# Performance work log

Measured on AMD Instinct MI355X. Metric: run time of the kernel, lower is better.

Reference implementation:

```python
import jax, jax.numpy as jnp
import numpy as np

STRIDE = 3


def _conv_block(x, W, b):
    # x: (B, L, C) -> windows (B, L-2, 3C) via fixed-stride slicing (faithful to scan_conv)
    B, L, C = x.shape
    Lw = L - STRIDE + 1
    win = jnp.concatenate([x[:, i:Lw + i, :] for i in range(STRIDE)], axis=-1)  # (B, Lw, 3C)
    y = jax.nn.leaky_relu(jnp.einsum('blk,ok->blo', win, W) + b)  # torch Linear: x @ W.T + b
    # zero_gate: zero rows of the *window* tensor zero the output
    mask = (jnp.sum(win, axis=2, keepdims=True) != 0).astype(y.dtype)
    y = y * mask
    # max_pool1d over sequence, kernel=2 stride=2 (floor)
    Lp = y.shape[1] // 2
    y = y[:, :2 * Lp, :].reshape(B, Lp, 2, -1).max(axis=2)
    return y


def setup_inputs() -> dict:
    key = jax.random.key(0)
    ks = jax.random.split(key, 16)
    B, PAD, E, IMG, V = 1024, 30, 512, 2048, 32000
    c1, c2, c3, lin2 = 200, 300, 300, 400
    lin1_in = 2 * c3 + IMG  # flattened (B,2,300) + image -> 600 + 2048
    s = 0.02
    return {
        'image_vectors': jax.random.normal(ks[0], (B, IMG), jnp.float32),
        'sentences': jax.random.randint(ks[1], (B, PAD), 0, V, jnp.int32),
        'embed_table': jax.random.normal(ks[2], (V, E), jnp.float32),
        'W1': jax.random.normal(ks[3], (c1, E * STRIDE), jnp.float32) * s,
        'b1': jnp.zeros((c1,), jnp.float32),
        'W2': jax.random.normal(ks[4], (c2, c1 * STRIDE), jnp.float32) * s,
        'b2': jnp.zeros((c2,), jnp.float32),
        'W3': jax.random.normal(ks[5], (c3, c2 * STRIDE), jnp.float32) * s,
        'b3': jnp.zeros((c3,), jnp.float32),
        'Wm': jax.random.normal(ks[6], (lin2, lin1_in), jnp.float32) * s,
        'bm': jnp.zeros((lin2,), jnp.float32),
        'Wo': jax.random.normal(ks[7], (1, lin2), jnp.float32) * s,
        'bo': jnp.zeros((1,), jnp.float32),
    }


def reference(image_vectors, sentences, embed_table, W1, b1, W2, b2, W3, b3, Wm, bm, Wo, bo):
    x = embed_table[sentences]                       # (B, 30, 512)
    x = _conv_block(x, W1, b1)                       # (B, 14, 200)
    x = _conv_block(x, W2, b2)                       # (B, 6, 300)
    x = _conv_block(x, W3, b3)                       # (B, 2, 300)
    B = x.shape[0]
    feats = jnp.concatenate([x.reshape(B, -1), image_vectors], axis=1)  # (B, 2648)
    h = jax.nn.leaky_relu(feats @ Wm.T + bm)         # (B, 400)
    out = h @ Wo.T + bo                              # (B, 1)
    return out
```

## Files before the change

### kernel.cpp

```cpp
#include <hip/hip_runtime.h>
#include <hip/hip_bf16.h>

#define LEAKY(v) ((v) > 0.0f ? (v) : 0.01f * (v))

constexpr int B_   = 1024;
constexpr int PAD  = 30;
constexpr int E    = 512;
constexpr int IMG  = 2048;
constexpr int C1   = 200;
constexpr int C2   = 300;
constexpr int C3   = 300;
constexpr int LIN2 = 400;

constexpr int NT1P = 16, KT1 = 48;
constexpr int NT2P = 20, KT2 = 21;
constexpr int NT3P = 24, KT3 = 30;
constexpr int NTMP = 28, KTM = 83;
constexpr int FK  = 2656;

constexpr int T1 = NT1P * KT1;
constexpr int T2 = NT2P * KT2;
constexpr int T3 = NT3P * KT3;
constexpr int TM = NTMP * KTM;
constexpr int TTOT = T1 + T2 + T3 + TM;

typedef __attribute__((ext_vector_type(8))) short bf16x8;
typedef __attribute__((ext_vector_type(4))) float f32x4;

__device__ inline unsigned short f2bf(float f) {
    __hip_bfloat16 h = __float2bfloat16(f);
    return *reinterpret_cast<unsigned short*>(&h);
}
__device__ inline float bf2f(unsigned short u) {
    unsigned int b = ((unsigned int)u) << 16;
    return __uint_as_float(b);
}

__global__ __launch_bounds__(256) void convert_all(
    const float* __restrict__ W1, const float* __restrict__ W2,
    const float* __restrict__ W3, const float* __restrict__ Wm,
    unsigned short* __restrict__ W1t, unsigned short* __restrict__ W2t,
    unsigned short* __restrict__ W3t, unsigned short* __restrict__ Wmt)
{
    int idx = blockIdx.x * 256 + threadIdx.x;
    if (idx >= TTOT * 64) return;
    int lane = idx & 63, t = idx >> 6;
    unsigned short v[8];

    if (t < T1) {
        int kk = t % KT1, nt = t / KT1;
        int ch = nt * 16 + (lane & 15);
        int k0 = kk * 32 + (lane >> 4) * 8;
        #pragma unroll
        for (int j = 0; j < 8; ++j)
            v[j] = (ch < C1) ? f2bf(W1[(size_t)ch * (3*E) + k0 + j]) : (unsigned short)0;
        ushort4* dst = reinterpret_cast<ushort4*>(W1t) + (size_t)t * 128 + lane * 2;
        dst[0] = ushort4{v[0],v[1],v[2],v[3]};
        dst[1] = ushort4{v[4],v[5],v[6],v[7]};
    } else if (t < T1 + T2) {
        int tt = t - T1;
        int kk = tt % KT2, nt = tt / KT2;
        int ch = nt * 16 + (lane & 15);
        int rowoff = kk / 7;
        int cbase  = (kk % 7) * 32 + (lane >> 4) * 8;
        #pragma unroll
        for (int j = 0; j < 8; ++j) {
            int c = cbase + j;
            v[j] = (ch < C2 && c < C1) ? f2bf(W2[(size_t)ch * (3*C1) + rowoff * C1 + c])
                                       : (unsigned short)0;
        }
        ushort4* dst = reinterpret_cast<ushort4*>(W2t) + (size_t)tt * 128 + lane * 2;
        dst[0] = ushort4{v[0],v[1],v[2],v[3]};
        dst[1] = ushort4{v[4],v[5],v[6],v[7]};
    } else if (t < T1 + T2 + T3) {
        int tt = t - T1 - T2;
        int kk = tt % KT3, nt = tt / KT3;
        int ch = nt * 16 + (lane & 15);
        int rowoff = kk / 10;
        int cbase  = (kk % 10) * 32 + (lane >> 4) * 8;
        #pragma unroll
        for (int j = 0; j < 8; ++j) {
            int c = cbase + j;
            v[j] = (ch < C3 && c < C2) ? f2bf(W3[(size_t)ch * (3*C2) + rowoff * C2 + c])
                                       : (unsigned short)0;
        }
        ushort4* dst = reinterpret_cast<ushort4*>(W3t) + (size_t)tt * 128 + lane * 2;
        dst[0] = ushort4{v[0],v[1],v[2],v[3]};
        dst[1] = ushort4{v[4],v[5],v[6],v[7]};
    } else {
        int tt = t - T1 - T2 - T3;
        int kk = tt % KTM, nt = tt / KTM;
        int ch = nt * 16 + (lane & 15);
        int kbase = kk * 32 + (lane >> 4) * 8;
        #pragma unroll
        for (int j = 0; j < 8; ++j) {
            int k = kbase + j;
            v[j] = (ch < LIN2 && k < 2648) ? f2bf(Wm[(size_t)ch * 2648 + k])
                                           : (unsigned short)0;
        }
        ushort4* dst = reinterpret_cast<ushort4*>(Wmt) + (size_t)tt * 128 + lane * 2;
        dst[0] = ushort4{v[0],v[1],v[2],v[3]};
        dst[1] = ushort4{v[4],v[5],v[6],v[7]};
    }
}

__global__ __launch_bounds__(512, 4) void conv_fused(
    const int* __restrict__ sent, const float* __restrict__ emb,
    const unsigned short* __restrict__ W1t, const float* __restrict__ b1,
    const unsigned short* __restrict__ W2t, const float* __restrict__ b2,
    const unsigned short* __restrict__ W3t, const float* __restrict__ b3,
    const float* __restrict__ image, unsigned short* __restrict__ feats)
{
    const int blk = blockIdx.x;
    const int tid = threadIdx.x;
    __shared__ unsigned short xs[66 * 256];
    __shared__ float rs[64];
    __shared__ float rs2[36];
    __shared__ float rs3[12];
    char* xsb = reinterpret_cast<char*>(xs);

    const int wid = tid >> 6, lane = tid & 63;
    const int kg = lane >> 4, trow = lane & 15, g = kg;

    const bf16x8* wb1 = reinterpret_cast<const bf16x8*>(W1t);
    const bf16x8* wp0 = wb1 + (size_t)((wid    ) * KT1) * 64 + lane;
    const bf16x8* wp1 = wb1 + (size_t)((wid + 8) * KT1) * 64 + lane;

    f32x4 c00={0,0,0,0},c01={0,0,0,0},c02={0,0,0,0},c03={0,0,0,0};
    f32x4 c10={0,0,0,0},c11={0,0,0,0},c12={0,0,0,0},c13={0,0,0,0};

    #pragma unroll
    for (int h = 0; h < 2; ++h) {
        if (h == 1) __syncthreads();

        #pragma unroll
        for (int r8 = 0; r8 < 8; ++r8) {
            int r = wid + 8 * r8;
            if (r < 60) {
                int bl = r / 30, rr = r % 30;
                int R = bl * 32 + rr;
                int row = sent[(2 * blk + bl) * PAD + rr];
                float4 e = reinterpret_cast<const float4*>(
                    emb + (size_t)row * E + h * 256)[lane];
                float sum = e.x + e.y + e.z + e.w;
                ushort4 pk4{f2bf(e.x), f2bf(e.y), f2bf(e.z), f2bf(e.w)};
                int c = lane >> 1;
                int bo = R * 512 + ((c ^ (R & 7)) << 4) + (lane & 1) * 8;
                *reinterpret_cast<ushort4*>(xsb + bo) = pk4;
                for (int off = 32; off; off >>= 1) sum += __shfl_down(sum, off);
                if (lane == 0) { if (h == 0) rs[R] = sum; else rs[R] += sum; }
            }
        }
        if (tid < 384) {
            int zi = tid >> 6;
            int R = (zi < 2) ? (30 + zi) : (60 + zi);
            int c = lane >> 1;
            int bo = R * 512 + ((c ^ (R & 7)) << 4) + (lane & 1) * 8;
            *reinterpret_cast<ushort4*>(xsb + bo) = ushort4{0,0,0,0};
        }
        if (h == 0 && tid < 4) {
            const int pr[4] = {30, 31, 62, 63};
            rs[pr[tid]] = 0.f;
        }
        __syncthreads();

        if (wid < 5) {
            #pragma unroll
            for (int rowoff = 0; rowoff < 3; ++rowoff) {
                const int R0 = trow + rowoff;
                const int R1 = R0 + 16, R2 = R0 + 32, R3 = R0 + 48;
                #pragma unroll
                for (int cc = 0; cc < 8; ++cc) {
                    const int kk = rowoff * 16 + h * 8 + cc;
                    const int ch2 = cc * 4 + kg;
                    bf16x8 a0 = *reinterpret_cast<const bf16x8*>(
                        xsb + R0 * 512 + (((ch2) ^ (R0 & 7)) << 4));
                    bf16x8 a1 = *reinterpret_cast<const bf16x8*>(
                        xsb + R1 * 512 + (((ch2) ^ (R1 & 7)) << 4));
                    bf16x8 a2 = *reinterpret_cast<const bf16x8*>(
                        xsb + R2 * 512 + (((ch2) ^ (R2 & 7)) << 4));
                    bf16x8 a3 = *reinterpret_cast<const bf16x8*>(
                        xsb + R3 * 512 + (((ch2) ^ (R3 & 7)) << 4));
                    bf16x8 b0 = wp0[kk * 64];
                    bf16x8 b1v = wp1[kk * 64];
                    c00 = __builtin_amdgcn_mfma_f32_16x16x32_bf16(a0, b0, c00, 0, 0, 0);
                    c01 = __builtin_amdgcn_mfma_f32_16x16x32_bf16(a1, b0, c01, 0, 0, 0);
                    c02 = __builtin_amdgcn_mfma_f32_16x16x32_bf16(a2, b0, c02, 0, 0, 0);
                    c03 = __builtin_amdgcn_mfma_f32_16x16x32_bf16(a3, b0, c03, 0, 0, 0);
                    c10 = __builtin_amdgcn_mfma_f32_16x16x32_bf16(a0, b1v, c10, 0, 0, 0);
                    c11 = __builtin_amdgcn_mfma_f32_16x16x32_bf16(a1, b1v, c11, 0, 0, 0);
                    c12 = __builtin_amdgcn_mfma_f32_16x16x32_bf16(a2, b1v, c12, 0, 0, 0);
                    c13 = __builtin_amdgcn_mfma_f32_16x16x32_bf16(a3, b1v, c13, 0, 0, 0);
                }
            }
        } else {
            #pragma unroll
            for (int rowoff = 0; rowoff < 3; ++rowoff) {
                const int R0 = trow + rowoff;
                const int R1 = R0 + 16, R2 = R0 + 32, R3 = R0 + 48;
                #pragma unroll
                for (int cc = 0; cc < 8; ++cc) {
                    const int kk = rowoff * 16 + h * 8 + cc;
                    const int ch2 = cc * 4 + kg;
                    bf16x8 a0 = *reinterpret_cast<const bf16x8*>(
                        xsb + R0 * 512 + (((ch2) ^ (R0 & 7)) << 4));
                    bf16x8 a1 = *reinterpret_cast<const bf16x8*>(
                        xsb + R1 * 512 + (((ch2) ^ (R1 & 7)) << 4));
                    bf16x8 a2 = *reinterpret_cast<const bf16x8*>(
                        xsb + R2 * 512 + (((ch2) ^ (R2 & 7)) << 4));
                    bf16x8 a3 = *reinterpret_cast<const bf16x8*>(
                        xsb + R3 * 512 + (((ch2) ^ (R3 & 7)) << 4));
                    bf16x8 b0 = wp0[kk * 64];
                    c00 = __builtin_amdgcn_mfma_f32_16x16x32_bf16(a0, b0, c00, 0, 0, 0);
                    c01 = __builtin_amdgcn_mfma_f32_16x16x32_bf16(a1, b0, c01, 0, 0, 0);
                    c02 = __builtin_amdgcn_mfma_f32_16x16x32_bf16(a2, b0, c02, 0, 0, 0);
                    c03 = __builtin_amdgcn_mfma_f32_16x16x32_bf16(a3, b0, c03, 0, 0, 0);
                }
            }
        }
    }
    __syncthreads();

    for (int idx = tid; idx < 36 * 32; idx += 512) {
        int r = idx >> 5, ck = idx & 31;
        union { ushort4 u4[2]; bf16x8 v; } pk;
        pk.u4[0] = ushort4{0,0,0,0}; pk.u4[1] = ushort4{0,0,0,0};
        *reinterpret_cast<bf16x8*>(xsb + r * 512 + (ck << 4)) = pk.v;
    }
    __syncthreads();

#define EPIM1(MT, CM) do {                                                       \
    int bl = (MT) >> 1;                                                          \
    int mloc = ((MT) & 1) * 16;                                                  \
    _Pragma("unroll")                                                            \
    for (int hf = 0; hf < 2; ++hf) {                                             \
        int wl = mloc + 4 * g + 2 * hf;                                          \
        int tp = wl >> 1;                                                        \
        if (tp < 14) {                                                           \
            float v0 = CM[2*hf] + bia, v1 = CM[2*hf+1] + bia;                    \
            v0 = LEAKY(v0); v1 = LEAKY(v1);                                      \
            int rb = bl * 32 + wl;                                               \
            if (rs[rb] + rs[rb+1] + rs[rb+2] == 0.f) v0 = 0.f;                   \
            if (rs[rb+1] + rs[rb+2] + rs[rb+3] == 0.f) v1 = 0.f;                 \
            int rg = bl * 18 + tp;                                               \
            int bo = rg * 512 + ((((ch) >> 3) ^ (rg & 7)) << 4) + ((ch) & 7) * 2;\
            *reinterpret_cast<unsigned short*>(xsb + bo) = f2bf(fmaxf(v0, v1));  \
        }                                                                        \
    }                                                                            \
} while (0)

#define EPI1(NTI, CA, CB, CC, CD) do {                                           \
    int ch = (wid + 8 * (NTI)) * 16 + trow;                                      \
    if (ch < C1) {                                                               \
        float bia = b1[ch];                                                      \
        EPIM1(0, CA); EPIM1(1, CB); EPIM1(2, CC); EPIM1(3, CD);                  \
    }                                                                            \
} while (0)

    EPI1(0, c00, c01, c02, c03);
    if (wid < 5) {
        EPI1(1, c10, c11, c12, c13);
    }
#undef EPI1
#undef EPIM1
    __syncthreads();

    for (int r = wid; r < 36; r += 8) {
        float s = 0.f;
        #pragma unroll
        for (int j = 0; j < 4; ++j) {
            int e = lane + 64 * j;
            int chunk = e >> 3, within = e & 7;
            s += bf2f(*reinterpret_cast<unsigned short*>(
                xsb + r * 512 + ((chunk ^ (r & 7)) << 4) + within * 2));
        }
        for (int off = 32; off; off >>= 1) s += __shfl_down(s, off);
        if (lane == 0) rs2[r] = s;
    }
    __syncthreads();

    const bf16x8* wb2 = reinterpret_cast<const bf16x8*>(W2t);
    const int nt2a = wid, nt2b = wid + 8;
    const int nt2c = (wid + 16 < NT2P) ? (wid + 16) : (NT2P - 1);
    const bf16x8* q0 = wb2 + (size_t)(nt2a * KT2) * 64 + lane;
    const bf16x8* q1 = wb2 + (size_t)(nt2b * KT2) * 64 + lane;
    const bf16x8* q2 = wb2 + (size_t)(nt2c * KT2) * 64 + lane;

    f32x4 d00={0,0,0,0},d01={0,0,0,0};
    f32x4 d10={0,0,0,0},d11={0,0,0,0};
    f32x4 d20={0,0,0,0},d21={0,0,0,0};

    {
        int kidx = 0;
        #pragma unroll
        for (int rowoff = 0; rowoff < 3; ++rowoff) {
            const int R0 = trow + rowoff;
            const int R1 = R0 + 18;
            const int b3_0 = R0 * 512 + (((R0 & 7) ^ kg) << 4);
            const int b3_1 = R1 * 512 + (((R1 & 7) ^ kg) << 4);
            #pragma unroll
            for (int cc = 0; cc < 7; ++cc, ++kidx) {
                bf16x8 a0 = *reinterpret_cast<const bf16x8*>(xsb + (b3_0 ^ (cc << 6)));
                bf16x8 a1 = *reinterpret_cast<const bf16x8*>(xsb + (b3_1 ^ (cc << 6)));
                bf16x8 b0 = q0[kidx * 64];
                bf16x8 b1v = q1[kidx * 64];
                bf16x8 b2v = q2[kidx * 64];
                d00 = __builtin_amdgcn_mfma_f32_16x16x32_bf16(a0, b0,  d00, 0, 0, 0);
                d01 = __builtin_amdgcn_mfma_f32_16x16x32_bf16(a1, b0,  d01, 0, 0, 0);
                d10 = __builtin_amdgcn_mfma_f32_16x16x32_bf16(a0, b1v, d10, 0, 0, 0);
                d11 = __builtin_amdgcn_mfma_f32_16x16x32_bf16(a1, b1v, d11, 0, 0, 0);
                d20 = __builtin_amdgcn_mfma_f32_16x16x32_bf16(a0, b2v, d20, 0, 0, 0);
                d21 = __builtin_amdgcn_mfma_f32_16x16x32_bf16(a1, b2v, d21, 0, 0, 0);
            }
        }
    }
    __syncthreads();

    for (int idx = tid; idx < 15 * 40; idx += 512) {
        int r = idx / 40, ck = idx % 40;
        union { ushort4 u4[2]; bf16x8 v; } pk;
        pk.u4[0] = ushort4{0,0,0,0}; pk.u4[1] = ushort4{0,0,0,0};
        *reinterpret_cast<bf16x8*>(xsb + r * 640 + (ck << 4)) = pk.v;
    }
    __syncthreads();

#define EPI2F(NT, DA, DB) do {                                                   \
    int ch = (NT) * 16 + trow;                                                   \
    if (ch < C2) {                                                               \
        float bia = b2[ch];                                                      \
        _Pragma("unroll")                                                        \
        for (int hf = 0; hf < 2; ++hf) {                                         \
            int t0 = 4 * g + 2 * hf;                                             \
            if (t0 < 12) {                                                       \
                { float v0 = LEAKY(DA[2*hf]   + bia);                            \
                  float v1 = LEAKY(DA[2*hf+1] + bia);                            \
                  if (rs2[t0] + rs2[t0+1] + rs2[t0+2] == 0.f) v0 = 0.f;          \
                  if (rs2[t0+1] + rs2[t0+2] + rs2[t0+3] == 0.f) v1 = 0.f;        \
                  int rg = (t0 >> 1);                                            \
                  int bo = rg * 640 + ((((ch)>>3) ^ (rg & 7)) << 4) + ((ch)&7)*2;\
                  *reinterpret_cast<unsigned short*>(xsb + bo) = f2bf(fmaxf(v0, v1)); } \
                { float v0 = LEAKY(DB[2*hf]   + bia);                            \
                  float v1 = LEAKY(DB[2*hf+1] + bia);                            \
                  int rb = 18 + t0;                                              \
                  if (rs2[rb] + rs2[rb+1] + rs2[rb+2] == 0.f) v0 = 0.f;          \
                  if (rs2[rb+1] + rs2[rb+2] + rs2[rb+3] == 0.f) v1 = 0.f;        \
                  int rg = 6 + (t0 >> 1);                                        \
                  int bo = rg * 640 + ((((ch)>>3) ^ (rg & 7)) << 4) + ((ch)&7)*2;\
                  *reinterpret_cast<unsigned short*>(xsb + bo) = f2bf(fmaxf(v0, v1)); } \
            }                                                                    \
        }                                                                        \
    }                                                                            \
} while (0)

    EPI2F(nt2a, d00, d01);
    EPI2F(nt2b, d10, d11);
    EPI2F(nt2c, d20, d21);
#undef EPI2F
    __syncthreads();

    for (int r = wid; r < 12; r += 8) {
        float s = 0.f;
        #pragma unroll
        for (int j = 0; j < 5; ++j) {
            int e = lane + 64 * j;
            int chunk = e >> 3, within = e & 7;
            s += bf2f(*reinterpret_cast<unsigned short*>(
                xsb + r * 640 + ((chunk ^ (r & 7)) << 4) + within * 2));
        }
        for (int off = 32; off; off >>= 1) s += __shfl_down(s, off);
        if (lane == 0) rs3[r] = s;
    }
    __syncthreads();

    const int rbase = (trow < 8) ? (6 * (trow >> 2) + (trow & 3)) : 12;

    const bf16x8* wb3 = reinterpret_cast<const bf16x8*>(W3t);
    const int nt3a = wid, nt3b = wid + 8;
    const int nt3c = (wid < 3) ? (wid + 16) : 19;
    const bf16x8* p0 = wb3 + (size_t)(nt3a * KT3) * 64 + lane;
    const bf16x8* p1 = wb3 + (size_t)(nt3b * KT3) * 64 + lane;
    const bf16x8* p2 = wb3 + (size_t)(nt3c * KT3) * 64 + lane;

    f32x4 e0={0,0,0,0},e1={0,0,0,0},e2={0,0,0,0};

    {
        int kidx = 0;
        #pragma unroll
        for (int rowoff = 0; rowoff < 3; ++rowoff) {
            const int R0 = rbase + rowoff;
            #pragma unroll
            for (int cc = 0; cc < 10; ++cc, ++kidx) {
                int chunk = cc * 4 + kg;
                bf16x8 a0 = *reinterpret_cast<const bf16x8*>(
                    xsb + R0 * 640 + ((chunk ^ (R0 & 7)) << 4));
                bf16x8 b0 = p0[kidx * 64];
                bf16x8 b1v = p1[kidx * 64];
                bf16x8 b2v = p2[kidx * 64];
                e0 = __builtin_amdgcn_mfma_f32_16x16x32_bf16(a0, b0,  e0, 0, 0, 0);
                e1 = __builtin_amdgcn_mfma_f32_16x16x32_bf16(a0, b1v, e1, 0, 0, 0);
                e2 = __builtin_amdgcn_mfma_f32_16x16x32_bf16(a0, b2v, e2, 0, 0, 0);
            }
        }
    }

#define EPI3F(NT, EM) do {                                                       \
    int ch = (NT) * 16 + trow;                                                   \
    if (ch < C3 && g < 2) {                                                      \
        float bia = b3[ch];                                                      \
        _Pragma("unroll")                                                        \
        for (int tp = 0; tp < 2; ++tp) {                                         \
            int rb = g * 6 + 2 * tp;                                             \
            float v0 = LEAKY(EM[2*tp]   + bia);                                  \
            float v1 = LEAKY(EM[2*tp+1] + bia);                                  \
            if (rs3[rb] + rs3[rb+1] + rs3[rb+2] == 0.f) v0 = 0.f;                \
            if (rs3[rb+1] + rs3[rb+2] + rs3[rb+3] == 0.f) v1 = 0.f;              \
            feats[(size_t)(2 * blk + g) * FK + tp * C3 + ch] = f2bf(fmaxf(v0, v1)); \
        }                                                                        \
    }                                                                            \
} while (0)

    EPI3F(nt3a, e0);
    EPI3F(nt3b, e1);
    EPI3F(nt3c, e2);
#undef EPI3F

    for (int idx = tid; idx < 2 * 257; idx += 512) {
        int bl = idx / 257, c = idx % 257;
        int b = 2 * blk + bl;
        if (c < 256) {
            const float4* src = reinterpret_cast<const float4*>(
                image + (size_t)b * IMG + c * 8);
            float4 a = src[0], d = src[1];
            ushort4* dst = reinterpret_cast<ushort4*>(feats + (size_t)b * FK + 600 + c * 8);
            dst[0] = ushort4{f2bf(a.x),f2bf(a.y),f2bf(a.z),f2bf(a.w)};
            dst[1] = ushort4{f2bf(d.x),f2bf(d.y),f2bf(d.z),f2bf(d.w)};
        } else {
            ushort4* dst = reinterpret_cast<ushort4*>(feats + (size_t)b * FK + 2648);
            dst[0] = ushort4{0,0,0,0};
            dst[1] = ushort4{0,0,0,0};
        }
    }
}

__global__ __launch_bounds__(256) void final_mfma(
    const unsigned short* __restrict__ feats, const unsigned short* __restrict__ Wmt,
    const float* __restrict__ bm, float* __restrict__ h)
{
    const int tid = threadIdx.x;
    const int wid = tid >> 6, lane = tid & 63;
    const int gw = blockIdx.x * 4 + wid;
    const int mt = gw / 14, q = gw % 14;
    const int kg = lane >> 4, trow = lane & 15, g = kg;
    const int m0 = mt * 16;

    const bf16x8* ap = reinterpret_cast<const bf16x8*>(feats)
                       + (size_t)(m0 + trow) * (FK / 8) + kg;
    const bf16x8* wb = reinterpret_cast<const bf16x8*>(Wmt);
    const bf16x8* wp0 = wb + (size_t)((q     ) * KTM) * 64 + lane;
    const bf16x8* wp1 = wb + (size_t)((q + 14) * KTM) * 64 + lane;

    f32x4 c0 = {0,0,0,0}, c1 = {0,0,0,0};

    bf16x8 aA = ap[0],     aB = ap[4];
    bf16x8 b0A = wp0[0],   b1A = wp1[0];
    bf16x8 b0B = wp0[64],  b1B = wp1[64];
    for (int kk = 0; kk < KTM - 2; ++kk) {
        bf16x8 a = aA, b0 = b0A, b1 = b1A;
        aA = aB; b0A = b0B; b1A = b1B;
        aB  = ap [(kk + 2) * 4];
        b0B = wp0[(kk + 2) * 64];
        b1B = wp1[(kk + 2) * 64];
        c0 = __builtin_amdgcn_mfma_f32_16x16x32_bf16(a, b0, c0, 0, 0, 0);
        c1 = __builtin_amdgcn_mfma_f32_16x16x32_bf16(a, b1, c1, 0, 0, 0);
    }
    c0 = __builtin_amdgcn_mfma_f32_16x16x32_bf16(aA, b0A, c0, 0, 0, 0);
    c1 = __builtin_amdgcn_mfma_f32_16x16x32_bf16(aA, b1A, c1, 0, 0, 0);
    c0 = __builtin_amdgcn_mfma_f32_16x16x32_bf16(aB, b0B, c0, 0, 0, 0);
    c1 = __builtin_amdgcn_mfma_f32_16x16x32_bf16(aB, b1B, c1, 0, 0, 0);

#define EPIM(NT, CM) do {                                                        \
    int ch = (NT) * 16 + trow;                                                   \
    if (ch < LIN2) {                                                             \
        float bia = bm[ch];                                                      \
        _Pragma("unroll")                                                        \
        for (int reg = 0; reg < 4; ++reg) {                                      \
            float v = LEAKY(CM[reg] + bia);                                      \
            h[(size_t)(m0 + 4 * g + reg) * LIN2 + ch] = v;                       \
        }                                                                        \
    }                                                                            \
} while (0)

    EPIM(q,      c0);
    EPIM(q + 14, c1);
#undef EPIM
}

__global__ __launch_bounds__(256) void final_reduce(
    const float* __restrict__ h, const float* __restrict__ Wo,
    const float* __restrict__ bo, float* __restrict__ out)
{
    const int tid = threadIdx.x;
    const int wid = tid >> 6, lane = tid & 63;
    const int b = blockIdx.x * 4 + wid;
    float s = 0.f;
    #pragma unroll
    for (int j = 0; j < 7; ++j) {
        int o = lane + 64 * j;
        if (o < LIN2) s += h[(size_t)b * LIN2 + o] * Wo[o];
    }
    for (int off = 32; off; off >>= 1) s += __shfl_down(s, off);
    if (lane == 0) out[b] = s + bo[0];
}

extern "C" void kernel_launch(void* const* d_in, const int* in_sizes, int n_in,
                              void* d_out, int out_size, void* d_ws, size_t ws_size,
                              hipStream_t stream) {
    const float* image = (const float*)d_in[0];
    const int*   sent  = (const int*)  d_in[1];
    const float* emb   = (const float*)d_in[2];
    const float* W1    = (const float*)d_in[3];
    const float* b1    = (const float*)d_in[4];
    const float* W2    = (const float*)d_in[5];
    const float* b2    = (const float*)d_in[6];
    const float* W3    = (const float*)d_in[7];
    const float* b3    = (const float*)d_in[8];
    const float* Wm    = (const float*)d_in[9];
    const float* bm    = (const float*)d_in[10];
    const float* Wo    = (const float*)d_in[11];
    const float* bo    = (const float*)d_in[12];
    float* out = (float*)d_out;

    unsigned short* W1t = (unsigned short*)d_ws;
    unsigned short* W2t = W1t + (size_t)T1 * 512;
    unsigned short* W3t = W2t + (size_t)T2 * 512;
    unsigned short* Wmt = W3t + (size_t)T3 * 512;
    unsigned short* feats = Wmt + (size_t)TM * 512;
    float* h = (float*)(feats + (size_t)B_ * FK);

    convert_all<<<(TTOT * 64 + 255) / 256, 256, 0, stream>>>(
        W1, W2, W3, Wm, W1t, W2t, W3t, Wmt);

    conv_fused<<<B_ / 2, 512, 0, stream>>>(
        sent, emb, W1t, b1, W2t, b2, W3t, b3, image, feats);

    final_mfma<<<224, 256, 0, stream>>>(feats, Wmt, bm, h);
    final_reduce<<<B_ / 4, 256, 0, stream>>>(h, Wo, bo, out);
}
```

Before: 98.41 us.

## Process one batch element per conv block instead of two

The fused conv kernel now handles a single sentence per workgroup and launches B blocks instead of B/2. Shared-memory tiles, accumulators and epilogues shrink to one batch row, so each block uses less LDS and fewer registers and the grid gets more parallelism. In exchange, each block reloads all conv weights for half as many rows, doubling weight traffic from L2, and the MFMA tiles are padded more (30 rows in 32, and in layer 3 only one of four row groups is useful).

```diff
diff --git a/kernel.cpp b/kernel.cpp
--- a/kernel.cpp
+++ b/kernel.cpp
@@ -111,12 +111,12 @@
     const unsigned short* __restrict__ W3t, const float* __restrict__ b3,
     const float* __restrict__ image, unsigned short* __restrict__ feats)
 {
-    const int blk = blockIdx.x;
+    const int bat = blockIdx.x;
     const int tid = threadIdx.x;
-    __shared__ unsigned short xs[66 * 256];
-    __shared__ float rs[64];
-    __shared__ float rs2[36];
-    __shared__ float rs3[12];
+    __shared__ unsigned short xs[34 * 256];
+    __shared__ float rs[32];
+    __shared__ float rs2[18];
+    __shared__ float rs3[9];
     char* xsb = reinterpret_cast<char*>(xs);
 
     const int wid = tid >> 6, lane = tid & 63;
@@ -126,20 +126,18 @@
     const bf16x8* wp0 = wb1 + (size_t)((wid    ) * KT1) * 64 + lane;
     const bf16x8* wp1 = wb1 + (size_t)((wid + 8) * KT1) * 64 + lane;
 
-    f32x4 c00={0,0,0,0},c01={0,0,0,0},c02={0,0,0,0},c03={0,0,0,0};
-    f32x4 c10={0,0,0,0},c11={0,0,0,0},c12={0,0,0,0},c13={0,0,0,0};
+    f32x4 c00={0,0,0,0},c01={0,0,0,0};
+    f32x4 c10={0,0,0,0},c11={0,0,0,0};
 
     #pragma unroll
     for (int h = 0; h < 2; ++h) {
         if (h == 1) __syncthreads();
 
         #pragma unroll
-        for (int r8 = 0; r8 < 8; ++r8) {
-            int r = wid + 8 * r8;
-            if (r < 60) {
-                int bl = r / 30, rr = r % 30;
-                int R = bl * 32 + rr;
-                int row = sent[(2 * blk + bl) * PAD + rr];
+        for (int r8 = 0; r8 < 4; ++r8) {
+            int R = wid + 8 * r8;
+            if (R < 30) {
+                int row = sent[bat * PAD + R];
                 float4 e = reinterpret_cast<const float4*>(
                     emb + (size_t)row * E + h * 256)[lane];
                 float sum = e.x + e.y + e.z + e.w;
@@ -151,77 +149,59 @@
                 if (lane == 0) { if (h == 0) rs[R] = sum; else rs[R] += sum; }
             }
         }
-        if (tid < 384) {
-            int zi = tid >> 6;
-            int R = (zi < 2) ? (30 + zi) : (60 + zi);
+        if (tid < 256) {
+            int R = 30 + (tid >> 6);
             int c = lane >> 1;
             int bo = R * 512 + ((c ^ (R & 7)) << 4) + (lane & 1) * 8;
             *reinterpret_cast<ushort4*>(xsb + bo) = ushort4{0,0,0,0};
         }
-        if (h == 0 && tid < 4) {
-            const int pr[4] = {30, 31, 62, 63};
-            rs[pr[tid]] = 0.f;
-        }
+        if (h == 0 && tid < 2) rs[30 + tid] = 0.f;
         __syncthreads();
 
         if (wid < 5) {
             #pragma unroll
             for (int rowoff = 0; rowoff < 3; ++rowoff) {
                 const int R0 = trow + rowoff;
-                const int R1 = R0 + 16, R2 = R0 + 32, R3 = R0 + 48;
+                const int R1 = R0 + 16;
                 #pragma unroll
                 for (int cc = 0; cc < 8; ++cc) {
                     const int kk = rowoff * 16 + h * 8 + cc;
                     const int ch2 = cc * 4 + kg;
                     bf16x8 a0 = *reinterpret_cast<const bf16x8*>(
-                        xsb + R0 * 512 + (((ch2) ^ (R0 & 7)) << 4));
+                        xsb + R0 * 512 + ((ch2 ^ (R0 & 7)) << 4));
                     bf16x8 a1 = *reinterpret_cast<const bf16x8*>(
-                        xsb + R1 * 512 + (((ch2) ^ (R1 & 7)) << 4));
-                    bf16x8 a2 = *reinterpret_cast<const bf16x8*>(
-                        xsb + R2 * 512 + (((ch2) ^ (R2 & 7)) << 4));
-                    bf16x8 a3 = *reinterpret_cast<const bf16x8*>(
-                        xsb + R3 * 512 + (((ch2) ^ (R3 & 7)) << 4));
+                        xsb + R1 * 512 + ((ch2 ^ (R1 & 7)) << 4));
                     bf16x8 b0 = wp0[kk * 64];
                     bf16x8 b1v = wp1[kk * 64];
                     c00 = __builtin_amdgcn_mfma_f32_16x16x32_bf16(a0, b0, c00, 0, 0, 0);
                     c01 = __builtin_amdgcn_mfma_f32_16x16x32_bf16(a1, b0, c01, 0, 0, 0);
-                    c02 = __builtin_amdgcn_mfma_f32_16x16x32_bf16(a2, b0, c02, 0, 0, 0);
-                    c03 = __builtin_amdgcn_mfma_f32_16x16x32_bf16(a3, b0, c03, 0, 0, 0);
                     c10 = __builtin_amdgcn_mfma_f32_16x16x32_bf16(a0, b1v, c10, 0, 0, 0);
                     c11 = __builtin_amdgcn_mfma_f32_16x16x32_bf16(a1, b1v, c11, 0, 0, 0);
-                    c12 = __builtin_amdgcn_mfma_f32_16x16x32_bf16(a2, b1v, c12, 0, 0, 0);
-                    c13 = __builtin_amdgcn_mfma_f32_16x16x32_bf16(a3, b1v, c13, 0, 0, 0);
                 }
             }
         } else {
             #pragma unroll
             for (int rowoff = 0; rowoff < 3; ++rowoff) {
                 const int R0 = trow + rowoff;
-                const int R1 = R0 + 16, R2 = R0 + 32, R3 = R0 + 48;
+                const int R1 = R0 + 16;
                 #pragma unroll
                 for (int cc = 0; cc < 8; ++cc) {
                     const int kk = rowoff * 16 + h * 8 + cc;
                     const int ch2 = cc * 4 + kg;
                     bf16x8 a0 = *reinterpret_cast<const bf16x8*>(
-                        xsb + R0 * 512 + (((ch2) ^ (R0 & 7)) << 4));
+                        xsb + R0 * 512 + ((ch2 ^ (R0 & 7)) << 4));
                     bf16x8 a1 = *reinterpret_cast<const bf16x8*>(
-                        xsb + R1 * 512 + (((ch2) ^ (R1 & 7)) << 4));
-                    bf16x8 a2 = *reinterpret_cast<const bf16x8*>(
-                        xsb + R2 * 512 + (((ch2) ^ (R2 & 7)) << 4));
-                    bf16x8 a3 = *reinterpret_cast<const bf16x8*>(
-                        xsb + R3 * 512 + (((ch2) ^ (R3 & 7)) << 4));
+                        xsb + R1 * 512 + ((ch2 ^ (R1 & 7)) << 4));
                     bf16x8 b0 = wp0[kk * 64];
                     c00 = __builtin_amdgcn_mfma_f32_16x16x32_bf16(a0, b0, c00, 0, 0, 0);
                     c01 = __builtin_amdgcn_mfma_f32_16x16x32_bf16(a1, b0, c01, 0, 0, 0);
-                    c02 = __builtin_amdgcn_mfma_f32_16x16x32_bf16(a2, b0, c02, 0, 0, 0);
-                    c03 = __builtin_amdgcn_mfma_f32_16x16x32_bf16(a3, b0, c03, 0, 0, 0);
                 }
             }
         }
     }
     __syncthreads();
 
-    for (int idx = tid; idx < 36 * 32; idx += 512) {
+    for (int idx = tid; idx < 18 * 32; idx += 512) {
         int r = idx >> 5, ck = idx & 31;
         union { ushort4 u4[2]; bf16x8 v; } pk;
         pk.u4[0] = ushort4{0,0,0,0}; pk.u4[1] = ushort4{0,0,0,0};
@@ -230,8 +210,7 @@
     __syncthreads();
 
 #define EPIM1(MT, CM) do {                                                       \
-    int bl = (MT) >> 1;                                                          \
-    int mloc = ((MT) & 1) * 16;                                                  \
+    int mloc = (MT) * 16;                                                        \
     _Pragma("unroll")                                                            \
     for (int hf = 0; hf < 2; ++hf) {                                             \
         int wl = mloc + 4 * g + 2 * hf;                                          \
@@ -239,33 +218,32 @@
         if (tp < 14) {                                                           \
             float v0 = CM[2*hf] + bia, v1 = CM[2*hf+1] + bia;                    \
             v0 = LEAKY(v0); v1 = LEAKY(v1);                                      \
-            int rb = bl * 32 + wl;                                               \
-            if (rs[rb] + rs[rb+1] + rs[rb+2] == 0.f) v0 = 0.f;                   \
-            if (rs[rb+1] + rs[rb+2] + rs[rb+3] == 0.f) v1 = 0.f;                 \
-            int rg = bl * 18 + tp;                                               \
+            if (rs[wl] + rs[wl+1] + rs[wl+2] == 0.f) v0 = 0.f;                   \
+            if (rs[wl+1] + rs[wl+2] + rs[wl+3] == 0.f) v1 = 0.f;                 \
+            int rg = tp;                                                         \
             int bo = rg * 512 + ((((ch) >> 3) ^ (rg & 7)) << 4) + ((ch) & 7) * 2;\
             *reinterpret_cast<unsigned short*>(xsb + bo) = f2bf(fmaxf(v0, v1));  \
         }                                                                        \
     }                                                                            \
 } while (0)
 
-#define EPI1(NTI, CA, CB, CC, CD) do {                                           \
+#define EPI1(NTI, CA, CB) do {                                                   \
     int ch = (wid + 8 * (NTI)) * 16 + trow;                                      \
     if (ch < C1) {                                                               \
         float bia = b1[ch];                                                      \
-        EPIM1(0, CA); EPIM1(1, CB); EPIM1(2, CC); EPIM1(3, CD);                  \
+        EPIM1(0, CA); EPIM1(1, CB);                                              \
     }                                                                            \
 } while (0)
 
-    EPI1(0, c00, c01, c02, c03);
+    EPI1(0, c00, c01);
     if (wid < 5) {
-        EPI1(1, c10, c11, c12, c13);
+        EPI1(1, c10, c11);
     }
 #undef EPI1
 #undef EPIM1
     __syncthreads();
 
-    for (int r = wid; r < 36; r += 8) {
+    for (int r = wid; r < 18; r += 8) {
         float s = 0.f;
         #pragma unroll
         for (int j = 0; j < 4; ++j) {
@@ -286,37 +264,29 @@
     const bf16x8* q1 = wb2 + (size_t)(nt2b * KT2) * 64 + lane;
     const bf16x8* q2 = wb2 + (size_t)(nt2c * KT2) * 64 + lane;
 
-    f32x4 d00={0,0,0,0},d01={0,0,0,0};
-    f32x4 d10={0,0,0,0},d11={0,0,0,0};
-    f32x4 d20={0,0,0,0},d21={0,0,0,0};
+    f32x4 d0={0,0,0,0},d1={0,0,0,0},d2={0,0,0,0};
 
     {
         int kidx = 0;
         #pragma unroll
         for (int rowoff = 0; rowoff < 3; ++rowoff) {
             const int R0 = trow + rowoff;
-            const int R1 = R0 + 18;
             const int b3_0 = R0 * 512 + (((R0 & 7) ^ kg) << 4);
-            const int b3_1 = R1 * 512 + (((R1 & 7) ^ kg) << 4);
             #pragma unroll
             for (int cc = 0; cc < 7; ++cc, ++kidx) {
                 bf16x8 a0 = *reinterpret_cast<const bf16x8*>(xsb + (b3_0 ^ (cc << 6)));
-                bf16x8 a1 = *reinterpret_cast<const bf16x8*>(xsb + (b3_1 ^ (cc << 6)));
                 bf16x8 b0 = q0[kidx * 64];
                 bf16x8 b1v = q1[kidx * 64];
                 bf16x8 b2v = q2[kidx * 64];
-                d00 = __builtin_amdgcn_mfma_f32_16x16x32_bf16(a0, b0,  d00, 0, 0, 0);
-                d01 = __builtin_amdgcn_mfma_f32_16x16x32_bf16(a1, b0,  d01, 0, 0, 0);
-                d10 = __builtin_amdgcn_mfma_f32_16x16x32_bf16(a0, b1v, d10, 0, 0, 0);
-                d11 = __builtin_amdgcn_mfma_f32_16x16x32_bf16(a1, b1v, d11, 0, 0, 0);
-                d20 = __builtin_amdgcn_mfma_f32_16x16x32_bf16(a0, b2v, d20, 0, 0, 0);
-                d21 = __builtin_amdgcn_mfma_f32_16x16x32_bf16(a1, b2v, d21, 0, 0, 0);
+                d0 = __builtin_amdgcn_mfma_f32_16x16x32_bf16(a0, b0,  d0, 0, 0, 0);
+                d1 = __builtin_amdgcn_mfma_f32_16x16x32_bf16(a0, b1v, d1, 0, 0, 0);
+                d2 = __builtin_amdgcn_mfma_f32_16x16x32_bf16(a0, b2v, d2, 0, 0, 0);
             }
         }
     }
     __syncthreads();
 
-    for (int idx = tid; idx < 15 * 40; idx += 512) {
+    for (int idx = tid; idx < 9 * 40; idx += 512) {
         int r = idx / 40, ck = idx % 40;
         union { ushort4 u4[2]; bf16x8 v; } pk;
         pk.u4[0] = ushort4{0,0,0,0}; pk.u4[1] = ushort4{0,0,0,0};
@@ -324,7 +294,7 @@
     }
     __syncthreads();
 
-#define EPI2F(NT, DA, DB) do {                                                   \
+#define EPI2F(NT, DM) do {                                                       \
     int ch = (NT) * 16 + trow;                                                   \
     if (ch < C2) {                                                               \
         float bia = b2[ch];                                                      \
@@ -332,33 +302,26 @@
         for (int hf = 0; hf < 2; ++hf) {                                         \
             int t0 = 4 * g + 2 * hf;                                             \
             if (t0 < 12) {                                                       \
-                { float v0 = LEAKY(DA[2*hf]   + bia);                            \
-                  float v1 = LEAKY(DA[2*hf+1] + bia);                            \
-                  if (rs2[t0] + rs2[t0+1] + rs2[t0+2] == 0.f) v0 = 0.f;          \
-                  if (rs2[t0+1] + rs2[t0+2] + rs2[t0+3] == 0.f) v1 = 0.f;        \
-                  int rg = (t0 >> 1);                                            \
-                  int bo = rg * 640 + ((((ch)>>3) ^ (rg & 7)) << 4) + ((ch)&7)*2;\
-                  *reinterpret_cast<unsigned short*>(xsb + bo) = f2bf(fmaxf(v0, v1)); } \
-                { float v0 = LEAKY(DB[2*hf]   + bia);                            \
-                  float v1 = LEAKY(DB[2*hf+1] + bia);                            \
-                  int rb = 18 + t0;                                              \
-                  if (rs2[rb] + rs2[rb+1] + rs2[rb+2] == 0.f) v0 = 0.f;          \
-                  if (rs2[rb+1] + rs2[rb+2] + rs2[rb+3] == 0.f) v1 = 0.f;        \
-                  int rg = 6 + (t0 >> 1);                                        \
-                  int bo = rg * 640 + ((((ch)>>3) ^ (rg & 7)) << 4) + ((ch)&7)*2;\
-                  *reinterpret_cast<unsigned short*>(xsb + bo) = f2bf(fmaxf(v0, v1)); } \
+                float v0 = LEAKY(DM[2*hf]   + bia);                              \
+                float v1 = LEAKY(DM[2*hf+1] + bia);                              \
+                if (rs2[t0] + rs2[t0+1] + rs2[t0+2] == 0.f) v0 = 0.f;            \
+                if (rs2[t0+1] + rs2[t0+2] + rs2[t0+3] == 0.f) v1 = 0.f;          \
+                int rg = (t0 >> 1);                                              \
+                int bo = rg * 640 + ((((ch)>>3) ^ (rg & 7)) << 4) + ((ch)&7)*2;  \
+                *reinterpret_cast<unsigned short*>(xsb + bo) = f2bf(fmaxf(v0, v1)); \
             }                                                                    \
         }                                                                        \
     }                                                                            \
 } while (0)
 
-    EPI2F(nt2a, d00, d01);
-    EPI2F(nt2b, d10, d11);
-    EPI2F(nt2c, d20, d21);
+    EPI2F(nt2a, d0);
+    EPI2F(nt2b, d1);
+    EPI2F(nt2c, d2);
 #undef EPI2F
     __syncthreads();
 
-    for (int r = wid; r < 12; r += 8) {
+    if (wid < 6) {
+        int r = wid;
         float s = 0.f;
         #pragma unroll
         for (int j = 0; j < 5; ++j) {
@@ -370,9 +333,10 @@
         for (int off = 32; off; off >>= 1) s += __shfl_down(s, off);
         if (lane == 0) rs3[r] = s;
     }
-    __syncthreads();
-
-    const int rbase = (trow < 8) ? (6 * (trow >> 2) + (trow & 3)) : 12;
+    if (tid >= 384 && tid < 387) rs3[6 + (tid - 384)] = 0.f;
+    __syncthreads();
+
+    const int rbase = (trow < 4) ? trow : 6;
 
     const bf16x8* wb3 = reinterpret_cast<const bf16x8*>(W3t);
     const int nt3a = wid, nt3b = wid + 8;
@@ -405,16 +369,16 @@
 
 #define EPI3F(NT, EM) do {                                                       \
     int ch = (NT) * 16 + trow;                                                   \
-    if (ch < C3 && g < 2) {                                                      \
+    if (ch < C3 && g == 0) {                                                     \
         float bia = b3[ch];                                                      \
         _Pragma("unroll")                                                        \
         for (int tp = 0; tp < 2; ++tp) {                                         \
-            int rb = g * 6 + 2 * tp;                                             \
+            int rb = 2 * tp;                                                     \
             float v0 = LEAKY(EM[2*tp]   + bia);                                  \
             float v1 = LEAKY(EM[2*tp+1] + bia);                                  \
             if (rs3[rb] + rs3[rb+1] + rs3[rb+2] == 0.f) v0 = 0.f;                \
             if (rs3[rb+1] + rs3[rb+2] + rs3[rb+3] == 0.f) v1 = 0.f;              \
-            feats[(size_t)(2 * blk + g) * FK + tp * C3 + ch] = f2bf(fmaxf(v0, v1)); \
+            feats[(size_t)bat * FK + tp * C3 + ch] = f2bf(fmaxf(v0, v1));        \
         }                                                                        \
     }                                                                            \
 } while (0)
@@ -424,18 +388,16 @@
     EPI3F(nt3c, e2);
 #undef EPI3F
 
-    for (int idx = tid; idx < 2 * 257; idx += 512) {
-        int bl = idx / 257, c = idx % 257;
-        int b = 2 * blk + bl;
-        if (c < 256) {
+    if (tid < 257) {
+        if (tid < 256) {
             const float4* src = reinterpret_cast<const float4*>(
-                image + (size_t)b * IMG + c * 8);
+                image + (size_t)bat * IMG + tid * 8);
             float4 a = src[0], d = src[1];
-            ushort4* dst = reinterpret_cast<ushort4*>(feats + (size_t)b * FK + 600 + c * 8);
+            ushort4* dst = reinterpret_cast<ushort4*>(feats + (size_t)bat * FK + 600 + tid * 8);
             dst[0] = ushort4{f2bf(a.x),f2bf(a.y),f2bf(a.z),f2bf(a.w)};
             dst[1] = ushort4{f2bf(d.x),f2bf(d.y),f2bf(d.z),f2bf(d.w)};
         } else {
-            ushort4* dst = reinterpret_cast<ushort4*>(feats + (size_t)b * FK + 2648);
+            ushort4* dst = reinterpret_cast<ushort4*>(feats + (size_t)bat * FK + 2648);
             dst[0] = ushort4{0,0,0,0};
             dst[1] = ushort4{0,0,0,0};
         }
@@ -540,7 +502,7 @@
     convert_all<<<(TTOT * 64 + 255) / 256, 256, 0, stream>>>(
         W1, W2, W3, Wm, W1t, W2t, W3t, Wmt);
 
-    conv_fused<<<B_ / 2, 512, 0, stream>>>(
+    conv_fused<<<B_, 512, 0, stream>>>(
         sent, emb, W1t, b1, W2t, b2, W3t, b3, image, feats);
 
     final_mfma<<<224, 256, 0, stream>>>(feats, Wmt, bm, h);
```

After: 128.9 us. 1.31x slower.
